# Kernel optimization log

Measured on AMD Instinct MI355X. Metric: run time of the kernel, lower is better.

## Reference

```python
import jax, jax.numpy as jnp
import numpy as np

P_SIZES = (1, 2, 4)
O_SIZE = 32
EPS = 1e-5


def bilin_matrix(S, O):
    """Interpolation matrix (O, S) for torch UpsamplingBilinear2d (align_corners=True)."""
    if S == 1:
        return jnp.ones((O, 1), dtype=jnp.float32)
    pos = jnp.arange(O, dtype=jnp.float32) * ((S - 1) / (O - 1))
    lo = jnp.clip(jnp.floor(pos).astype(jnp.int32), 0, S - 2)
    frac = pos - lo.astype(jnp.float32)
    rows = jnp.arange(O)
    M = jnp.zeros((O, S), dtype=jnp.float32)
    M = M.at[rows, lo].add(1.0 - frac).at[rows, lo + 1].add(frac)
    return M


def setup_inputs() -> dict:
    key = jax.random.key(0)
    ks = jax.random.split(key, 12)
    n, C, H = 16, 512, 32
    c4 = C // 4      # 128, value/pyramid channels
    qk = c4 // 8     # 16, query/key channels inside SAE
    s = 0.05
    return {
        "x": jax.random.normal(ks[0], (n, C, H, H), jnp.float32),
        "rce_w": jax.random.normal(ks[1], (3, c4, C), jnp.float32) * s,   # 1x1 conv per pyramid scale
        "rce_b": jax.random.normal(ks[2], (3, c4), jnp.float32) * s,
        "q_w": jax.random.normal(ks[3], (qk, c4), jnp.float32) * s,       # SAE query 1x1 conv
        "q_b": jax.random.normal(ks[4], (qk,), jnp.float32) * s,
        "k_w": jax.random.normal(ks[5], (qk, c4), jnp.float32) * s,       # SAE key 1x1 conv
        "k_b": jax.random.normal(ks[6], (qk,), jnp.float32) * s,
        "value_w": jax.random.normal(ks[7], (c4, C), jnp.float32) * s,    # value 1x1 conv
        "value_b": jax.random.normal(ks[8], (c4,), jnp.float32) * s,
        "fusion_w": jax.random.normal(ks[9], (C, 3 * c4, 3, 3), jnp.float32) * s,  # 3x3 conv, no bias
        "bn_scale": 1.0 + jax.random.normal(ks[10], (C,), jnp.float32) * s,
        "bn_bias": jax.random.normal(ks[11], (C,), jnp.float32) * s,
        "gamma": jnp.asarray(0.5, jnp.float32),
    }


def reference(x, rce_w, rce_b, q_w, q_b, k_w, k_b, value_w, value_b,
              fusion_w, bn_scale, bn_bias, gamma):
    n, C, H, W = x.shape
    c4 = C // 4
    L = H * W

    # value projection: 1x1 conv then flatten -> (n, c4, L)
    proj_value = (jnp.einsum('oc,nchw->nohw', value_w, x)
                  + value_b[None, :, None, None]).reshape(n, c4, L)

    outs = []
    for i, sz in enumerate(P_SIZES):
        # AdaptiveAvgPool2d((sz, sz)) with divisible input -> exact uniform pooling
        pooled = x.reshape(n, C, sz, H // sz, sz, W // sz).mean(axis=(3, 5))
        # 1x1 conv C -> c4
        feat = jnp.einsum('oc,ncij->noij', rce_w[i], pooled) + rce_b[i][None, :, None, None]
        # bilinear upsample (align_corners=True) to (O_SIZE, O_SIZE)
        M = bilin_matrix(sz, O_SIZE)
        up = jnp.einsum('oi,pj,ncij->ncop', M, M, feat)  # (n, c4, H, W)
        # SAE: query/key 1x1 convs, flatten, bmm + softmax
        q = (jnp.einsum('oc,nchw->nohw', q_w, up) + q_b[None, :, None, None]).reshape(n, -1, L)
        k = (jnp.einsum('oc,nchw->nohw', k_w, up) + k_b[None, :, None, None]).reshape(n, -1, L)
        energy = jnp.einsum('ncl,ncm->nlm', q, k)        # (n, L, L)
        attn = jax.nn.softmax(energy, axis=-1)
        # temp = bmm(value, attn^T): temp[c,m] = sum_l value[c,l] * attn[m,l]
        outs.append(jnp.einsum('ncl,nml->ncm', proj_value, attn).reshape(n, c4, H, W))

    cat = jnp.concatenate(outs, axis=1)                  # (n, 3*c4, H, W)
    y = jax.lax.conv_general_dilated(
        cat, fusion_w, window_strides=(1, 1), padding=((1, 1), (1, 1)),
        dimension_numbers=('NCHW', 'OIHW', 'NCHW'))
    # BatchNorm2d in training mode (default): batch statistics over (N, H, W)
    mean = y.mean(axis=(0, 2, 3))
    var = y.var(axis=(0, 2, 3))
    y = (y - mean[None, :, None, None]) * (bn_scale / jnp.sqrt(var + EPS))[None, :, None, None] \
        + bn_bias[None, :, None, None]
    y = jax.nn.relu(y)
    return gamma * y + x
```

## Files before the change

kernel.cpp:

```cpp
#include <hip/hip_runtime.h>
#include <hip/hip_fp16.h>
#include <math.h>

#define OFF_COR   0u
#define OFF_PVH   2097152u
#define OFF_Y     3145728u
#define OFF_CATP  11534336u
#define OFF_QH    15085568u
#define OFF_KH    15347712u
#define OFF_POOL  16134144u
#define OFF_FEAT  16297984u
#define OFF_AW    16338944u
#define OFF_MEANS 17223680u
#define OFF_STAT  17225728u
#define OFF_VWH   17226752u

typedef __bf16 bf16x8 __attribute__((ext_vector_type(8)));
typedef _Float16 f16x8 __attribute__((ext_vector_type(8)));
typedef _Float16 f16x4 __attribute__((ext_vector_type(4)));
typedef float f32x4 __attribute__((ext_vector_type(4)));

__device__ __forceinline__ unsigned short f2bf(float f) {
  unsigned int u = __float_as_uint(f);
  unsigned int r = u + 0x7fff + ((u >> 16) & 1);
  return (unsigned short)(r >> 16);
}

__device__ __forceinline__ unsigned short f2h(float f) {
  union { _Float16 h; unsigned short u; } cv;
  cv.h = (_Float16)f;
  return cv.u;
}

__device__ __forceinline__ void gload_lds16(const void* g, void* l) {
  __builtin_amdgcn_global_load_lds(
      (const __attribute__((address_space(1))) unsigned int*)g,
      (__attribute__((address_space(3))) unsigned int*)l, 16, 0, 0);
}

__global__ __launch_bounds__(256) void pool_kernel(const float* __restrict__ x,
                                                   float* __restrict__ pool) {
  int b = blockIdx.x;
  int t = threadIdx.x;
  const float4* xp = (const float4*)(x + (size_t)b * 1024);
  float4 v = xp[t];
  float s4 = v.x + v.y + v.z + v.w;
  __shared__ float sm[256];
  __shared__ float p4s[16];
  sm[t] = s4;
  __syncthreads();
  if (t < 16) {
    int br = t >> 2, bc = t & 3;
    float s = 0.f;
#pragma unroll
    for (int rr = 0; rr < 8; ++rr) {
      int base = br * 64 + rr * 8 + bc * 2;
      s += sm[base] + sm[base + 1];
    }
    s *= (1.f / 64.f);
    p4s[t] = s;
    pool[(size_t)b * 20 + t] = s;
  }
  __syncthreads();
  if (t < 4) {
    int i2 = t >> 1, j2 = t & 1;
    float s = (p4s[(2*i2)*4 + 2*j2]     + p4s[(2*i2)*4 + 2*j2 + 1] +
               p4s[(2*i2+1)*4 + 2*j2]   + p4s[(2*i2+1)*4 + 2*j2 + 1]) * 0.25f;
    pool[(size_t)b * 20 + 16 + t] = s;
  }
}

__global__ __launch_bounds__(64) void feat_kernel(const float* __restrict__ pool,
                                                  const float* __restrict__ rce_w,
                                                  const float* __restrict__ rce_b,
                                                  float* __restrict__ feat) {
  int o = blockIdx.x, n = blockIdx.y, t = threadIdx.x;
  float part[20];
#pragma unroll
  for (int j = 0; j < 20; ++j) part[j] = 0.f;
  for (int c = t; c < 512; c += 64) {
    const float* pl = pool + ((size_t)n * 512 + c) * 20;
    float w2 = rce_w[(size_t)(128 + o) * 512 + c];
    float w4 = rce_w[(size_t)(256 + o) * 512 + c];
#pragma unroll
    for (int j = 0; j < 4; ++j)  part[j]     += w2 * pl[16 + j];
#pragma unroll
    for (int j = 0; j < 16; ++j) part[4 + j] += w4 * pl[j];
  }
  __shared__ float red[64][20];
#pragma unroll
  for (int j = 0; j < 20; ++j) red[t][j] = part[j];
  __syncthreads();
  if (t < 20) {
    float s = 0.f;
    for (int i = 0; i < 64; ++i) s += red[i][t];
    s += (t < 4) ? rce_b[128 + o] : rce_b[256 + o];
    feat[((size_t)n * 128 + o) * 20 + t] = s;
  }
}

__global__ __launch_bounds__(256) void qk2_kernel(const float* __restrict__ feat,
                                                  const float* __restrict__ q_w,
                                                  const float* __restrict__ q_b,
                                                  const float* __restrict__ k_w,
                                                  const float* __restrict__ k_b,
                                                  unsigned short* __restrict__ qh,
                                                  unsigned short* __restrict__ kh) {
  int n = blockIdx.x, t = threadIdx.x;
  __shared__ float fL[128 * 20];
  __shared__ float GH[2][16][20];
  for (int idx = t; idx < 2560; idx += 256) fL[idx] = feat[(size_t)n * 2560 + idx];
  __syncthreads();
  for (int idx = t; idx < 640; idx += 256) {
    int which = idx / 320, rem = idx % 320, qc = rem / 20, j = rem % 20;
    const float* w = which ? k_w : q_w;
    float s = which ? k_b[qc] : q_b[qc];
    for (int c = 0; c < 128; ++c) s += w[qc * 128 + c] * fL[c * 20 + j];
    GH[which][qc][j] = s;
  }
  __syncthreads();
  for (int it = 0; it < 16; ++it) {
    int row = t + 256 * it;
    int l = row & 1023, which = (row >> 10) & 1, s = row >> 11;
    int ry = l >> 5, cx = l & 31;
    int t0, t1, t2, t3;
    float w0, w1, w2, w3;
    if (s == 0) {
      float a = ry * (1.0f / 31.0f), b = cx * (1.0f / 31.0f);
      t0 = 0; t1 = 1; t2 = 2; t3 = 3;
      w0 = (1.f - a) * (1.f - b); w1 = (1.f - a) * b;
      w2 = a * (1.f - b);         w3 = a * b;
    } else {
      float pr = ry * (3.0f / 31.0f);
      int lr = (int)pr; if (lr > 2) lr = 2;
      float fr = pr - (float)lr;
      float pc = cx * (3.0f / 31.0f);
      int lc = (int)pc; if (lc > 2) lc = 2;
      float fc = pc - (float)lc;
      int base = 4 + lr * 4 + lc;
      t0 = base; t1 = base + 1; t2 = base + 4; t3 = base + 5;
      w0 = (1.f - fr) * (1.f - fc); w1 = (1.f - fr) * fc;
      w2 = fr * (1.f - fc);         w3 = fr * fc;
    }
    float val[16];
#pragma unroll
    for (int qc = 0; qc < 16; ++qc) {
      const float* G = GH[which][qc];
      val[qc] = w0 * G[t0] + w1 * G[t1] + w2 * G[t2] + w3 * G[t3];
    }
    unsigned short* dst = (which ? kh : qh) + (((size_t)(s * 16 + n) * 1024 + l) * 16);
#pragma unroll
    for (int u = 0; u < 4; ++u)
      *(ushort4*)(dst + 4 * u) = make_ushort4(f2h(val[4*u]), f2h(val[4*u+1]),
                                              f2h(val[4*u+2]), f2h(val[4*u+3]));
  }
}

__global__ __launch_bounds__(256) void xcast_kernel(const float* __restrict__ x,
                                                    unsigned short* __restrict__ xT) {
  int lt = blockIdx.x, ct = blockIdx.y, n = blockIdx.z;
  int l0 = lt * 64, c0 = ct * 64, t = threadIdx.x;
  __shared__ float tile[64 * 65];
#pragma unroll
  for (int i = 0; i < 16; ++i) {
    int idx = t + 256 * i;
    int c = idx >> 6, l = idx & 63;
    tile[c * 65 + l] = x[((size_t)n * 512 + c0 + c) * 1024 + l0 + l];
  }
  __syncthreads();
#pragma unroll
  for (int i = 0; i < 16; ++i) {
    int idx = t + 256 * i;
    int l = idx >> 6, c = idx & 63;
    xT[((size_t)n * 1024 + l0 + l) * 512 + c0 + c] = f2h(tile[c * 65 + l]);
  }
}

__global__ __launch_bounds__(256) void vwcast_kernel(const float* __restrict__ vw,
                                                     unsigned short* __restrict__ vwh) {
  int i = blockIdx.x * 256 + threadIdx.x;
  vwh[i] = f2h(vw[i]);
}

__global__ __launch_bounds__(256) void pvmm2_kernel(const unsigned short* __restrict__ vwh,
                                                    const unsigned short* __restrict__ xT,
                                                    const float* __restrict__ vb,
                                                    unsigned short* __restrict__ pvh) {
  int l0 = blockIdx.x * 64;
  int n = blockIdx.y;
  int t = threadIdx.x, lane = t & 63, wv = t >> 6;
  int wm = (wv & 1) * 64, wn = (wv >> 1) * 32;

  __shared__ short Asm[128 * 32];
  __shared__ short Bsm[64 * 32];

  int ar0 = t >> 2,        aq0 = (t & 3) ^ ((ar0 >> 1) & 3);
  int idx1 = t + 256; int ar1 = idx1 >> 2, aq1 = (idx1 & 3) ^ ((ar1 >> 1) & 3);
  int br  = t >> 2,        bq  = (t & 3) ^ ((br >> 1) & 3);
  const unsigned short* Ab0 = vwh + (size_t)ar0 * 512 + aq0 * 8;
  const unsigned short* Ab1 = vwh + (size_t)ar1 * 512 + aq1 * 8;
  const unsigned short* Bb  = xT + ((size_t)n * 1024 + l0 + br) * 512 + bq * 8;
  char* ldsA = (char*)Asm;
  char* ldsB = (char*)Bsm;
  int wvoff = wv * 1024;
  int r15 = lane & 15, kg = lane >> 4;
  int kq = kg ^ ((r15 >> 1) & 3);

  f32x4 acc[4][2];
#pragma unroll
  for (int i = 0; i < 4; ++i)
#pragma unroll
    for (int j = 0; j < 2; ++j) acc[i][j] = (f32x4){0.f, 0.f, 0.f, 0.f};

  for (int k0 = 0; k0 < 512; k0 += 32) {
    __syncthreads();
    gload_lds16(Ab0 + k0, ldsA + wvoff);
    gload_lds16(Ab1 + k0, ldsA + 4096 + wvoff);
    gload_lds16(Bb + k0,  ldsB + wvoff);
    __syncthreads();
    f16x8 af[4], bfr[2];
#pragma unroll
    for (int mt2 = 0; mt2 < 4; ++mt2)
      af[mt2] = *(const f16x8*)&Asm[(wm + mt2 * 16 + r15) * 32 + kq * 8];
#pragma unroll
    for (int nt2 = 0; nt2 < 2; ++nt2)
      bfr[nt2] = *(const f16x8*)&Bsm[(wn + nt2 * 16 + r15) * 32 + kq * 8];
#pragma unroll
    for (int mt2 = 0; mt2 < 4; ++mt2)
#pragma unroll
      for (int nt2 = 0; nt2 < 2; ++nt2)
        acc[mt2][nt2] = __builtin_amdgcn_mfma_f32_16x16x32_f16(af[mt2], bfr[nt2], acc[mt2][nt2], 0, 0, 0);
  }

  int c_lo = wm + (lane >> 4) * 4;
  int l_lo = wn + (lane & 15);
#pragma unroll
  for (int mt2 = 0; mt2 < 4; ++mt2)
#pragma unroll
    for (int nt2 = 0; nt2 < 2; ++nt2) {
      int l = l0 + l_lo + nt2 * 16;
#pragma unroll
      for (int r = 0; r < 4; ++r) {
        int c = c_lo + mt2 * 16 + r;
        pvh[((size_t)n * 128 + c) * 1024 + l] = f2h(acc[mt2][nt2][r] + vb[c]);
      }
    }
}

__global__ __launch_bounds__(256) void mean_kernel(const unsigned short* __restrict__ pvh,
                                                   float* __restrict__ means) {
  int c = blockIdx.x, n = blockIdx.y, t = threadIdx.x;
  f16x4 v = ((const f16x4*)(pvh + ((size_t)n * 128 + c) * 1024))[t];
  float s = (float)v[0] + (float)v[1] + (float)v[2] + (float)v[3];
  for (int o = 32; o > 0; o >>= 1) s += __shfl_down(s, o);
  __shared__ float wsum[4];
  if ((t & 63) == 0) wsum[t >> 6] = s;
  __syncthreads();
  if (t == 0) means[n * 128 + c] = (wsum[0] + wsum[1] + wsum[2] + wsum[3]) * (1.f / 1024.f);
}

__global__ __launch_bounds__(64) void basecor_kernel(const float* __restrict__ means,
                                                     const float* __restrict__ fw,
                                                     float* __restrict__ cor) {
  int oc = blockIdx.x, n = blockIdx.y, t = threadIdx.x;
  float S[9];
#pragma unroll
  for (int j = 0; j < 9; ++j) S[j] = 0.f;
  for (int c = t; c < 128; c += 64) {
    float m = means[n * 128 + c];
    const float* wp = fw + (size_t)oc * 3456 + c * 9;
#pragma unroll
    for (int j = 0; j < 9; ++j) S[j] += m * wp[j];
  }
  __shared__ float red[64][9];
  __shared__ float Sf[9];
#pragma unroll
  for (int j = 0; j < 9; ++j) red[t][j] = S[j];
  __syncthreads();
  if (t < 9) {
    float s = 0.f;
    for (int i = 0; i < 64; ++i) s += red[i][t];
    Sf[t] = s;
  }
  __syncthreads();
  if (t < 9) {
    int a = t / 3, b = t % 3;
    float s = 0.f;
#pragma unroll
    for (int ky = 0; ky < 3; ++ky) {
      if ((a == 0 && ky == 0) || (a == 2 && ky == 2)) continue;
#pragma unroll
      for (int kx = 0; kx < 3; ++kx) {
        if ((b == 0 && kx == 0) || (b == 2 && kx == 2)) continue;
        s += Sf[ky * 3 + kx];
      }
    }
    cor[((size_t)n * 512 + oc) * 9 + t] = s;
  }
}

__global__ __launch_bounds__(128) void fillcat_kernel(unsigned short* __restrict__ catp) {
  int b = blockIdx.x;
  int n = b / 132, e = b % 132;
  int py, px;
  if (e < 34)       { py = 0;          px = e; }
  else if (e < 68)  { py = 33;         px = e - 34; }
  else if (e < 100) { py = e - 68 + 1; px = 0; }
  else              { py = e - 100 + 1; px = 33; }
  unsigned int* row = (unsigned int*)(catp + ((size_t)n * 1156 + py * 34 + px) * 256);
  row[threadIdx.x] = 0u;
}

__global__ __launch_bounds__(256) void wcast_kernel(const float* __restrict__ fw,
                                                    unsigned short* __restrict__ Aw) {
  int oc = blockIdx.x, t = threadIdx.x;
  for (int j = t; j < 2304; j += 256) {
    int g = j / 576, r = j % 576;
    int tap = r >> 6, i = r & 63;
    Aw[(size_t)oc * 2304 + j] =
        f2bf(fw[(size_t)oc * 3456 + (size_t)(128 + g * 64 + i) * 9 + tap]);
  }
}

__global__ __launch_bounds__(256) void fattn_kernel(const unsigned short* __restrict__ qh,
                                                    const unsigned short* __restrict__ kh,
                                                    const unsigned short* __restrict__ pvh,
                                                    unsigned short* __restrict__ catp) {
  int m0 = blockIdx.x * 64;
  int n = blockIdx.y, sc = blockIdx.z;
  int t = threadIdx.x, lane = t & 63, wv = t >> 6;
  int wc = (wv >> 1) * 64;
  int wm2 = (wv & 1) * 32;
  int r15 = lane & 15, kg = lane >> 4;
  int kq = kg ^ ((r15 >> 1) & 3);

  const unsigned short* qb  = qh + ((size_t)(sc * 16 + n) * 1024 + m0 + wv * 16) * 16;
  const unsigned short* kb  = kh + ((size_t)(sc * 16 + n) * 1024) * 16;
  const unsigned short* pvb = pvh + (size_t)n * 128 * 1024;

  __shared__ short PVs[2 * 128 * 32];
  __shared__ _Float16 Us[64 * 72];
  __shared__ float rsum[64];

  f16x8 zf = {0, 0, 0, 0, 0, 0, 0, 0};
  f16x8 qa = (kg < 2) ? *(const f16x8*)(qb + r15 * 16 + kg * 8) : zf;

  int prow = t >> 2;
  int aq = (t & 3) ^ ((prow >> 1) & 3);
  const unsigned short* Pb0 = pvb + (size_t)prow * 1024 + aq * 8;
  const unsigned short* Pb1 = pvb + (size_t)(prow + 64) * 1024 + aq * 8;
  char* ldsPV = (char*)PVs;
  int wvoff = wv * 1024;

  f32x4 acc[4][2];
#pragma unroll
  for (int i = 0; i < 4; ++i)
#pragma unroll
    for (int j = 0; j < 2; ++j) acc[i][j] = (f32x4){0.f, 0.f, 0.f, 0.f};
  float rs[4] = {0.f, 0.f, 0.f, 0.f};

  for (int it = 0; it < 16; ++it) {
    int l0 = it * 64;
    __syncthreads();
    gload_lds16(Pb0 + l0,      ldsPV + wvoff);
    gload_lds16(Pb1 + l0,      ldsPV + 4096 + wvoff);
    gload_lds16(Pb0 + l0 + 32, ldsPV + 8192 + wvoff);
    gload_lds16(Pb1 + l0 + 32, ldsPV + 12288 + wvoff);

    f32x4 sacc[4];
#pragma unroll
    for (int lt = 0; lt < 4; ++lt) {
      f16x8 kbf = (kg < 2)
        ? *(const f16x8*)(kb + (size_t)(l0 + lt * 16 + r15) * 16 + kg * 8) : zf;
      sacc[lt] = __builtin_amdgcn_mfma_f32_16x16x32_f16(qa, kbf, (f32x4){0.f,0.f,0.f,0.f}, 0, 0, 0);
    }
#pragma unroll
    for (int lt = 0; lt < 4; ++lt)
#pragma unroll
      for (int r = 0; r < 4; ++r) {
        float e = __expf(sacc[lt][r]);
        Us[(wv * 16 + kg * 4 + r) * 72 + lt * 16 + r15] = (_Float16)e;
        rs[r] += e;
      }
    __syncthreads();

#pragma unroll
    for (int ks = 0; ks < 2; ++ks) {
      f16x8 bfr[2];
#pragma unroll
      for (int nt = 0; nt < 2; ++nt)
        bfr[nt] = *(const f16x8*)&Us[(wm2 + nt * 16 + r15) * 72 + ks * 32 + kg * 8];
#pragma unroll
      for (int ct = 0; ct < 4; ++ct) {
        f16x8 af = *(const f16x8*)&PVs[ks * 4096 + (wc + ct * 16 + r15) * 32 + kq * 8];
#pragma unroll
        for (int nt = 0; nt < 2; ++nt)
          acc[ct][nt] = __builtin_amdgcn_mfma_f32_16x16x32_f16(af, bfr[nt], acc[ct][nt], 0, 0, 0);
      }
    }
  }

#pragma unroll
  for (int r = 0; r < 4; ++r) {
    rs[r] += __shfl_xor(rs[r], 1);
    rs[r] += __shfl_xor(rs[r], 2);
    rs[r] += __shfl_xor(rs[r], 4);
    rs[r] += __shfl_xor(rs[r], 8);
  }
  if (r15 == 0) {
#pragma unroll
    for (int r = 0; r < 4; ++r) rsum[wv * 16 + kg * 4 + r] = rs[r];
  }
  __syncthreads();

#pragma unroll
  for (int nt = 0; nt < 2; ++nt) {
    float inv = 1.f / rsum[wm2 + nt * 16 + r15];
    int pix = m0 + wm2 + nt * 16 + r15;
    unsigned short* ob = catp + ((size_t)n * 1156 + ((pix >> 5) + 1) * 34 + (pix & 31) + 1) * 256
                       + sc * 128 + wc + kg * 4;
#pragma unroll
    for (int ct = 0; ct < 4; ++ct) {
      ushort4 o = make_ushort4(f2bf(acc[ct][nt][0] * inv), f2bf(acc[ct][nt][1] * inv),
                               f2bf(acc[ct][nt][2] * inv), f2bf(acc[ct][nt][3] * inv));
      *(ushort4*)(ob + ct * 16) = o;
    }
  }
}

__global__ __launch_bounds__(256) void convmm_kernel(const unsigned short* __restrict__ Aw,
                                                     const unsigned short* __restrict__ catp,
                                                     const float* __restrict__ cor,
                                                     float* __restrict__ y) {
  int ntile = blockIdx.x;
  int n = ntile >> 3, y0 = (ntile & 7) * 4;
  int m0 = blockIdx.y * 128;
  int t = threadIdx.x;
  int lane = t & 63, wv = t >> 6;
  int wm = (wv & 1) * 64, wn = (wv >> 1) * 64;

  __shared__ short Asm[2 * 2 * 128 * 32];
  __shared__ short Bimg[208 * 64];

  int idx0 = t, idx1 = t + 256;
  int ar0 = idx0 >> 2, aq0 = (idx0 & 3) ^ ((ar0 >> 1) & 3);
  int ar1 = idx1 >> 2, aq1 = (idx1 & 3) ^ ((ar1 >> 1) & 3);
  size_t abase0 = (size_t)(m0 + ar0) * 2304 + aq0 * 8;
  size_t abase1 = (size_t)(m0 + ar1) * 2304 + aq1 * 8;
  char* ldsA = (char*)Asm;
  char* ldsB = (char*)Bimg;
  int wvoff = wv * 1024;

  const unsigned short* cb = catp + ((size_t)n * 1156 + (size_t)y0 * 34) * 256;
  int bpx = lane >> 3;
  int bch = (lane & 7) ^ (bpx & 7);

  int r15 = lane & 15, kg = lane >> 4;
  int kq = kg ^ ((r15 >> 1) & 3);

  int pxl[4];
#pragma unroll
  for (int nt = 0; nt < 4; ++nt) {
    int pn = wn + nt * 16 + r15;
    pxl[nt] = (pn >> 5) * 34 + (pn & 31);
  }

  f32x4 acc[4][4];
#pragma unroll
  for (int i = 0; i < 4; ++i)
#pragma unroll
    for (int j = 0; j < 4; ++j) acc[i][j] = (f32x4){0.f, 0.f, 0.f, 0.f};

  for (int j = wv; j < 26; j += 4)
    gload_lds16(cb + (size_t)(j * 8 + bpx) * 256 + bch * 8, ldsB + j * 1024);
  gload_lds16(Aw + abase0,      ldsA + wvoff);
  gload_lds16(Aw + abase1,      ldsA + 4096 + wvoff);
  gload_lds16(Aw + abase0 + 32, ldsA + 8192 + wvoff);
  gload_lds16(Aw + abase1 + 32, ldsA + 12288 + wvoff);
  __syncthreads();

  int q = 0;
  for (int g = 0; g < 4; ++g) {
    for (int tap = 0; tap < 9; ++tap, ++q) {
      char* la = ldsA + (q & 1) * 16384;
      if (q < 35) {
        int tapn = tap + 1, gn = g;
        if (tapn == 9) { tapn = 0; gn = g + 1; }
        size_t akk = (size_t)(gn * 576 + tapn * 64);
        char* ln = ldsA + ((q + 1) & 1) * 16384;
        gload_lds16(Aw + abase0 + akk,      ln + wvoff);
        gload_lds16(Aw + abase1 + akk,      ln + 4096 + wvoff);
        gload_lds16(Aw + abase0 + akk + 32, ln + 8192 + wvoff);
        gload_lds16(Aw + abase1 + akk + 32, ln + 12288 + wvoff);
      }
      int sy = tap / 3;
      int toff = sy * 34 + (tap - sy * 3);
#pragma unroll
      for (int c = 0; c < 2; ++c) {
        const short* As_ = (const short*)(la + c * 8192);
        bf16x8 af[4], bfv[4];
#pragma unroll
        for (int mt = 0; mt < 4; ++mt)
          af[mt] = *(const bf16x8*)&As_[(wm + mt * 16 + r15) * 32 + kq * 8];
#pragma unroll
        for (int nt = 0; nt < 4; ++nt) {
          int px = pxl[nt] + toff;
          int lch = (c * 4 + kg) ^ (px & 7);
          bfv[nt] = *(const bf16x8*)&Bimg[px * 64 + lch * 8];
        }
#pragma unroll
        for (int mt = 0; mt < 4; ++mt)
#pragma unroll
          for (int nt = 0; nt < 4; ++nt)
            acc[mt][nt] = __builtin_amdgcn_mfma_f32_16x16x32_bf16(af[mt], bfv[nt], acc[mt][nt], 0, 0, 0);
      }
      __syncthreads();
      if (tap == 8 && g < 3) {
        for (int j = wv; j < 26; j += 4)
          gload_lds16(cb + (size_t)(j * 8 + bpx) * 256 + (g + 1) * 64 + bch * 8,
                      ldsB + j * 1024);
        __syncthreads();
      }
    }
  }

  int pixbase = (ntile & 7) * 128 + wn + (lane & 15);
  int ocbase = m0 + wm + (lane >> 4) * 4;
#pragma unroll
  for (int mt = 0; mt < 4; ++mt)
#pragma unroll
    for (int nt = 0; nt < 4; ++nt) {
      int oc = ocbase + mt * 16;
      int pix = pixbase + nt * 16;
      int py = pix >> 5, px = pix & 31;
      int yc = (py == 0) ? 0 : ((py == 31) ? 2 : 1);
      int xc = (px == 0) ? 0 : ((px == 31) ? 2 : 1);
      const float* cp = cor + ((size_t)n * 512 + oc) * 9 + yc * 3 + xc;
      float* yp = y + ((size_t)n * 512 + oc) * 1024 + pix;
#pragma unroll
      for (int r = 0; r < 4; ++r) yp[(size_t)r * 1024] = acc[mt][nt][r] + cp[(size_t)r * 9];
    }
}

__global__ __launch_bounds__(256) void bnstat_kernel(const float* __restrict__ y,
                                                     const float* __restrict__ bn_scale,
                                                     const float* __restrict__ bn_bias,
                                                     float* __restrict__ stats) {
  int oc = blockIdx.x, t = threadIdx.x;
  float s = 0.f, ss = 0.f;
  for (int n = 0; n < 16; ++n) {
    float4 v = ((const float4*)(y + ((size_t)n * 512 + oc) * 1024))[t];
    s  += v.x + v.y + v.z + v.w;
    ss += v.x * v.x + v.y * v.y + v.z * v.z + v.w * v.w;
  }
  for (int o = 32; o > 0; o >>= 1) {
    s  += __shfl_down(s, o);
    ss += __shfl_down(ss, o);
  }
  __shared__ float rs[4], rss[4];
  if ((t & 63) == 0) { rs[t >> 6] = s; rss[t >> 6] = ss; }
  __syncthreads();
  if (t == 0) {
    float S = rs[0] + rs[1] + rs[2] + rs[3];
    float SS = rss[0] + rss[1] + rss[2] + rss[3];
    float mean = S * (1.f / 16384.f);
    float var = SS * (1.f / 16384.f) - mean * mean;
    float se = bn_scale[oc] / sqrtf(var + 1e-5f);
    stats[oc * 2] = se;
    stats[oc * 2 + 1] = bn_bias[oc] - mean * se;
  }
}

__global__ __launch_bounds__(256) void final_kernel(const float* __restrict__ y,
                                                    const float* __restrict__ x,
                                                    const float* __restrict__ stats,
                                                    const float* __restrict__ gamma,
                                                    float* __restrict__ outp) {
  int b = blockIdx.x;
  int c = b & 511;
  int t = threadIdx.x;
  float se = stats[c * 2], sh = stats[c * 2 + 1], g = gamma[0];
  float4 yv = ((const float4*)(y + (size_t)b * 1024))[t];
  float4 xv = ((const float4*)(x + (size_t)b * 1024))[t];
  float4 o;
  o.x = g * fmaxf(yv.x * se + sh, 0.f) + xv.x;
  o.y = g * fmaxf(yv.y * se + sh, 0.f) + xv.y;
  o.z = g * fmaxf(yv.z * se + sh, 0.f) + xv.z;
  o.w = g * fmaxf(yv.w * se + sh, 0.f) + xv.w;
  ((float4*)(outp + (size_t)b * 1024))[t] = o;
}

extern "C" void kernel_launch(void* const* d_in, const int* in_sizes, int n_in,
                              void* d_out, int out_size, void* d_ws, size_t ws_size,
                              hipStream_t stream) {
  const float* x        = (const float*)d_in[0];
  const float* rce_w    = (const float*)d_in[1];
  const float* rce_b    = (const float*)d_in[2];
  const float* q_w      = (const float*)d_in[3];
  const float* q_b      = (const float*)d_in[4];
  const float* k_w      = (const float*)d_in[5];
  const float* k_b      = (const float*)d_in[6];
  const float* value_w  = (const float*)d_in[7];
  const float* value_b  = (const float*)d_in[8];
  const float* fw       = (const float*)d_in[9];
  const float* bn_scale = (const float*)d_in[10];
  const float* bn_bias  = (const float*)d_in[11];
  const float* gamma    = (const float*)d_in[12];

  float* ws    = (float*)d_ws;
  float* cor   = ws + OFF_COR;
  unsigned short* pvh = (unsigned short*)(ws + OFF_PVH);
  float* ybuf  = ws + OFF_Y;
  unsigned short* xTbuf = (unsigned short*)(ws + OFF_Y);
  unsigned short* catp = (unsigned short*)(ws + OFF_CATP);
  unsigned short* qh   = (unsigned short*)(ws + OFF_QH);
  unsigned short* kh   = (unsigned short*)(ws + OFF_KH);
  float* pool  = ws + OFF_POOL;
  float* feat  = ws + OFF_FEAT;
  unsigned short* Aw = (unsigned short*)(ws + OFF_AW);
  float* means = ws + OFF_MEANS;
  float* stats = ws + OFF_STAT;
  unsigned short* vwh = (unsigned short*)(ws + OFF_VWH);
  float* outp  = (float*)d_out;

  hipLaunchKernelGGL(pool_kernel,    dim3(8192),       dim3(256), 0, stream, x, pool);
  hipLaunchKernelGGL(feat_kernel,    dim3(128, 16),    dim3(64),  0, stream, pool, rce_w, rce_b, feat);
  hipLaunchKernelGGL(qk2_kernel,     dim3(16),         dim3(256), 0, stream, feat, q_w, q_b, k_w, k_b, qh, kh);
  hipLaunchKernelGGL(xcast_kernel,   dim3(16, 8, 16),  dim3(256), 0, stream, x, xTbuf);
  hipLaunchKernelGGL(vwcast_kernel,  dim3(256),        dim3(256), 0, stream, value_w, vwh);
  hipLaunchKernelGGL(pvmm2_kernel,   dim3(16, 16),     dim3(256), 0, stream, vwh, xTbuf, value_b, pvh);
  hipLaunchKernelGGL(mean_kernel,    dim3(128, 16),    dim3(256), 0, stream, pvh, means);
  hipLaunchKernelGGL(basecor_kernel, dim3(512, 16),    dim3(64),  0, stream, means, fw, cor);
  hipLaunchKernelGGL(fillcat_kernel, dim3(2112),       dim3(128), 0, stream, catp);
  hipLaunchKernelGGL(wcast_kernel,   dim3(512),        dim3(256), 0, stream, fw, Aw);
  hipLaunchKernelGGL(fattn_kernel,   dim3(16, 16, 2),  dim3(256), 0, stream, qh, kh, pvh, catp);
  hipLaunchKernelGGL(convmm_kernel,  dim3(128, 4),     dim3(256), 0, stream, Aw, catp, cor, ybuf);
  hipLaunchKernelGGL(bnstat_kernel,  dim3(512),        dim3(256), 0, stream, ybuf, bn_scale, bn_bias, stats);
  hipLaunchKernelGGL(final_kernel,   dim3(8192),       dim3(256), 0, stream, ybuf, x, stats, gamma, outp);
}
```

Before: 259.3 us.

## Load conv weights directly to registers and double-buffer image tile in LDS

The fusion conv GEMM kernel stops staging the weight (A) tiles through shared memory. Each wave now loads its own A fragments from global memory straight into registers, double-buffered one tap ahead. The activation image tile in LDS is double-buffered across channel groups so the next group's load overlaps compute. This removes 35 per-tap block barriers, leaving one per group, at the cost of more VGPRs and uncoalesced, redundant global reads of weights across waves.

```diff
diff --git a/kernel.cpp b/kernel.cpp
--- a/kernel.cpp
+++ b/kernel.cpp
@@ -439,24 +439,16 @@
   int lane = t & 63, wv = t >> 6;
   int wm = (wv & 1) * 64, wn = (wv >> 1) * 64;
 
-  __shared__ short Asm[2 * 2 * 128 * 32];
-  __shared__ short Bimg[208 * 64];
-
-  int idx0 = t, idx1 = t + 256;
-  int ar0 = idx0 >> 2, aq0 = (idx0 & 3) ^ ((ar0 >> 1) & 3);
-  int ar1 = idx1 >> 2, aq1 = (idx1 & 3) ^ ((ar1 >> 1) & 3);
-  size_t abase0 = (size_t)(m0 + ar0) * 2304 + aq0 * 8;
-  size_t abase1 = (size_t)(m0 + ar1) * 2304 + aq1 * 8;
-  char* ldsA = (char*)Asm;
+  __shared__ short Bimg[2 * 208 * 64];
   char* ldsB = (char*)Bimg;
-  int wvoff = wv * 1024;
 
   const unsigned short* cb = catp + ((size_t)n * 1156 + (size_t)y0 * 34) * 256;
   int bpx = lane >> 3;
   int bch = (lane & 7) ^ (bpx & 7);
 
   int r15 = lane & 15, kg = lane >> 4;
-  int kq = kg ^ ((r15 >> 1) & 3);
+
+  const unsigned short* Ap = Aw + (size_t)(m0 + wm + r15) * 2304 + kg * 8;
 
   int pxl[4];
 #pragma unroll
@@ -471,56 +463,61 @@
 #pragma unroll
     for (int j = 0; j < 4; ++j) acc[i][j] = (f32x4){0.f, 0.f, 0.f, 0.f};
 
+  bf16x8 Ar[2][8];
+
   for (int j = wv; j < 26; j += 4)
     gload_lds16(cb + (size_t)(j * 8 + bpx) * 256 + bch * 8, ldsB + j * 1024);
-  gload_lds16(Aw + abase0,      ldsA + wvoff);
-  gload_lds16(Aw + abase1,      ldsA + 4096 + wvoff);
-  gload_lds16(Aw + abase0 + 32, ldsA + 8192 + wvoff);
-  gload_lds16(Aw + abase1 + 32, ldsA + 12288 + wvoff);
-  __syncthreads();
-
-  int q = 0;
+#pragma unroll
+  for (int c = 0; c < 2; ++c)
+#pragma unroll
+    for (int mt = 0; mt < 4; ++mt)
+      Ar[0][c * 4 + mt] = *(const bf16x8*)(Ap + (size_t)mt * 16 * 2304 + c * 32);
+  asm volatile("s_waitcnt vmcnt(0)" ::: "memory");
+  __builtin_amdgcn_s_barrier();
+
+#pragma unroll 2
   for (int g = 0; g < 4; ++g) {
-    for (int tap = 0; tap < 9; ++tap, ++q) {
-      char* la = ldsA + (q & 1) * 16384;
-      if (q < 35) {
-        int tapn = tap + 1, gn = g;
-        if (tapn == 9) { tapn = 0; gn = g + 1; }
-        size_t akk = (size_t)(gn * 576 + tapn * 64);
-        char* ln = ldsA + ((q + 1) & 1) * 16384;
-        gload_lds16(Aw + abase0 + akk,      ln + wvoff);
-        gload_lds16(Aw + abase1 + akk,      ln + 4096 + wvoff);
-        gload_lds16(Aw + abase0 + akk + 32, ln + 8192 + wvoff);
-        gload_lds16(Aw + abase1 + akk + 32, ln + 12288 + wvoff);
+    int gpar = g & 1;
+    if (g < 3) {
+      for (int j = wv; j < 26; j += 4)
+        gload_lds16(cb + (size_t)(j * 8 + bpx) * 256 + (g + 1) * 64 + bch * 8,
+                    ldsB + (gpar ^ 1) * 26624 + j * 1024);
+    }
+    const unsigned short* Agbase = Ap + g * 576;
+#pragma unroll
+    for (int tap = 0; tap < 9; ++tap) {
+      int par = (g + tap) & 1;
+      if (!(g == 3 && tap == 8)) {
+        const unsigned short* An = (tap == 8) ? (Agbase + 576) : (Agbase + (tap + 1) * 64);
+#pragma unroll
+        for (int c = 0; c < 2; ++c)
+#pragma unroll
+          for (int mt = 0; mt < 4; ++mt)
+            Ar[par ^ 1][c * 4 + mt] = *(const bf16x8*)(An + (size_t)mt * 16 * 2304 + c * 32);
       }
       int sy = tap / 3;
       int toff = sy * 34 + (tap - sy * 3);
-#pragma unroll
-      for (int c = 0; c < 2; ++c) {
-        const short* As_ = (const short*)(la + c * 8192);
-        bf16x8 af[4], bfv[4];
-#pragma unroll
-        for (int mt = 0; mt < 4; ++mt)
-          af[mt] = *(const bf16x8*)&As_[(wm + mt * 16 + r15) * 32 + kq * 8];
+      bf16x8 bfv[2][4];
+#pragma unroll
+      for (int c = 0; c < 2; ++c)
 #pragma unroll
         for (int nt = 0; nt < 4; ++nt) {
           int px = pxl[nt] + toff;
           int lch = (c * 4 + kg) ^ (px & 7);
-          bfv[nt] = *(const bf16x8*)&Bimg[px * 64 + lch * 8];
+          bfv[c][nt] = *(const bf16x8*)&Bimg[gpar * 13312 + px * 64 + lch * 8];
         }
 #pragma unroll
+      for (int c = 0; c < 2; ++c)
+#pragma unroll
         for (int mt = 0; mt < 4; ++mt)
 #pragma unroll
           for (int nt = 0; nt < 4; ++nt)
-            acc[mt][nt] = __builtin_amdgcn_mfma_f32_16x16x32_bf16(af[mt], bfv[nt], acc[mt][nt], 0, 0, 0);
-      }
-      __syncthreads();
-      if (tap == 8 && g < 3) {
-        for (int j = wv; j < 26; j += 4)
-          gload_lds16(cb + (size_t)(j * 8 + bpx) * 256 + (g + 1) * 64 + bch * 8,
-                      ldsB + j * 1024);
-        __syncthreads();
-      }
+            acc[mt][nt] = __builtin_amdgcn_mfma_f32_16x16x32_bf16(
+                Ar[par][c * 4 + mt], bfv[c][nt], acc[mt][nt], 0, 0, 0);
+    }
+    if (g < 3) {
+      asm volatile("s_waitcnt vmcnt(0)" ::: "memory");
+      __builtin_amdgcn_s_barrier();
     }
   }
 
```

New measurement: 317.8 us. +22.6%, slower.
